# Optimization experiments

Measured on AMD Instinct MI355X. Metric: run time of the kernel, lower is better.

## Reference

```python
import jax, jax.numpy as jnp
import numpy as np
from jax import lax

B_, L_, H_, P_ = 4, 8192, 1024, 64  # batch, seq, d_model, d_state//4
EPS = 1e-5


def setup_inputs() -> dict:
    key = jax.random.key(0)
    ks = jax.random.split(key, 20)
    s = 1.0 / np.sqrt(H_)
    inp = {
        "zH": jax.random.normal(ks[0], (B_, L_, H_), jnp.float32),
        "zL": jax.random.normal(ks[1], (B_, L_, H_), jnp.float32),
        "x": jax.random.normal(ks[2], (B_, L_, H_), jnp.float32),
        "t": jax.random.normal(ks[3], (B_, H_), jnp.float32),
        # AdaLN projections (d_model -> 2*d_model)
        "W_projH": jax.random.normal(ks[4], (H_, 2 * H_), jnp.float32) * s,
        "b_projH": jnp.zeros((2 * H_,), jnp.float32),
        "W_projL": jax.random.normal(ks[5], (H_, 2 * H_), jnp.float32) * s,
        "b_projL": jnp.zeros((2 * H_,), jnp.float32),
        # inj Linear (3*d_model -> d_model)
        "W_inj": jax.random.normal(ks[6], (3 * H_, H_), jnp.float32) * (1.0 / np.sqrt(3 * H_)),
        "b_inj": jnp.zeros((H_,), jnp.float32),
        # S5Dual params (diagonal complex SSM, bidirectional)
        "Lambda_re": -(0.1 + 0.4 * jax.random.uniform(ks[7], (P_,), jnp.float32)),
        "Lambda_im": jnp.pi * jnp.arange(P_, dtype=jnp.float32),
        "B_re": jax.random.normal(ks[8], (P_, H_), jnp.float32) * s,
        "B_im": jax.random.normal(ks[9], (P_, H_), jnp.float32) * s,
        "Cf_re": jax.random.normal(ks[10], (H_, P_), jnp.float32) * (1.0 / np.sqrt(P_)),
        "Cf_im": jax.random.normal(ks[11], (H_, P_), jnp.float32) * (1.0 / np.sqrt(P_)),
        "Cb_re": jax.random.normal(ks[12], (H_, P_), jnp.float32) * (1.0 / np.sqrt(P_)),
        "Cb_im": jax.random.normal(ks[13], (H_, P_), jnp.float32) * (1.0 / np.sqrt(P_)),
        "D": jax.random.normal(ks[14], (H_,), jnp.float32),
        "log_dt": jnp.log(0.001) + (jnp.log(0.1) - jnp.log(0.001)) * jax.random.uniform(ks[15], (P_,), jnp.float32),
    }
    return inp


def _adaln(x, cond, W, b):
    # x: [B,L,H], cond: [B,H]
    scale, shift = jnp.split(cond @ W + b, 2, axis=-1)
    mu = jnp.mean(x, axis=-1, keepdims=True)
    var = jnp.var(x, axis=-1, keepdims=True)
    xn = (x - mu) * lax.rsqrt(var + EPS)
    return xn * (1.0 + scale[:, None, :]) + shift[:, None, :]


def _binop(e1, e2):
    a1, b1 = e1
    a2, b2 = e2
    return a1 * a2, a2 * b1 + b2


def _s5_dual(u, Lambda_re, Lambda_im, B_re, B_im, Cf_re, Cf_im, Cb_re, Cb_im, D, log_dt):
    # u: [B,L,H] real -> [B,L,H] real. Bidirectional diagonal SSM (S5 style).
    Lam = Lambda_re + 1j * Lambda_im            # [P]
    dt = jnp.exp(log_dt)                        # [P]
    Lam_bar = jnp.exp(Lam * dt)                 # [P] ZOH discretization
    Bm = B_re + 1j * B_im                       # [P,H]
    B_bar = ((Lam_bar - 1.0) / Lam)[:, None] * Bm
    Bu = jnp.einsum('blh,ph->blp', u.astype(jnp.complex64), B_bar)  # [B,L,P]
    A = jnp.broadcast_to(Lam_bar, Bu.shape)
    xs_f = lax.associative_scan(_binop, (A, Bu), axis=1)[1]
    xs_b = jnp.flip(lax.associative_scan(_binop, (A, jnp.flip(Bu, axis=1)), axis=1)[1], axis=1)
    Cf = Cf_re + 1j * Cf_im
    Cb = Cb_re + 1j * Cb_im
    y = 2.0 * jnp.einsum('blp,hp->blh', xs_f, Cf).real \
        + 2.0 * jnp.einsum('blp,hp->blh', xs_b, Cb).real \
        + D * u
    return y


def reference(zH, zL, x, t, W_projH, b_projH, W_projL, b_projL, W_inj, b_inj,
              Lambda_re, Lambda_im, B_re, B_im, Cf_re, Cf_im, Cb_re, Cb_im, D, log_dt):
    zH = _adaln(zH, t, W_projH, b_projH)
    zL = _adaln(zL, t, W_projL, b_projL)
    h = jnp.concatenate([zH, zL, x], axis=-1)          # [B,L,3H]
    h = h @ W_inj + b_inj                              # [B,L,H]
    return _s5_dual(h, Lambda_re, Lambda_im, B_re, B_im, Cf_re, Cf_im, Cb_re, Cb_im, D, log_dt)
```

## Files before the change

kernel.cpp:

```cpp
#include <hip/hip_runtime.h>


#define LN_EPS 1e-5f

typedef __attribute__((ext_vector_type(8))) short bf16x8;
typedef __attribute__((ext_vector_type(8))) unsigned short u16x8;
typedef __attribute__((ext_vector_type(4))) float f32x4;

__device__ __forceinline__ unsigned short f2bf(float f) {
  unsigned int u = __float_as_uint(f);
  u += 0x7fffu + ((u >> 16) & 1u);
  return (unsigned short)(u >> 16);
}
__device__ __forceinline__ float bf2f(unsigned short s) {
  return __uint_as_float(((unsigned int)s) << 16);
}

__device__ __forceinline__ void gload16(const void* g, void* l) {
  __builtin_amdgcn_global_load_lds((const __attribute__((address_space(1))) void*)g,
                                   (__attribute__((address_space(3))) void*)l, 16, 0, 0);
}

__device__ __forceinline__ void phase_bar() {
  __builtin_amdgcn_sched_barrier(0);
  asm volatile("" ::: "memory");
  __builtin_amdgcn_s_barrier();
  __builtin_amdgcn_sched_barrier(0);
}

__global__ void proj_k(const float* __restrict__ t,
                       const float* __restrict__ WH, const float* __restrict__ bH,
                       const float* __restrict__ WL, const float* __restrict__ bL,
                       float* __restrict__ cond) {
  const int idx = blockIdx.x * 256 + threadIdx.x;
  const int tensor = idx >> 11;
  const int j2 = idx & 2047;
  const float* W = tensor ? WL : WH;
  const float bv = tensor ? bL[j2] : bH[j2];
  float a0 = bv, a1 = bv, a2 = bv, a3 = bv;
  #pragma unroll 4
  for (int k = 0; k < 1024; ++k) {
    const float w = W[k * 2048 + j2];
    a0 += t[k] * w; a1 += t[1024 + k] * w; a2 += t[2048 + k] * w; a3 += t[3072 + k] * w;
  }
  const int which = j2 >> 10, j = j2 & 1023;
  float* c = cond + (size_t)((tensor * 2 + which) * 4) * 1024 + j;
  c[0] = a0; c[1024] = a1; c[2048] = a2; c[3072] = a3;
}

__global__ void proj_part_k(const float* __restrict__ t,
                            const float* __restrict__ WH, const float* __restrict__ WL,
                            float* __restrict__ part) {
  const int bid = blockIdx.x;
  const int tensor = bid >> 7, ks = (bid >> 3) & 15, jc = bid & 7;
  const int j2 = jc * 256 + threadIdx.x;
  const float* W = tensor ? WL : WH;
  float a0 = 0.f, a1 = 0.f, a2 = 0.f, a3 = 0.f;
  const int k0 = ks * 64;
  #pragma unroll 4
  for (int k = k0; k < k0 + 64; ++k) {
    const float w = W[k * 2048 + j2];
    a0 += t[k] * w; a1 += t[1024 + k] * w; a2 += t[2048 + k] * w; a3 += t[3072 + k] * w;
  }
  float* p = part + ((size_t)(tensor * 16 + ks) * 4) * 2048 + j2;
  p[0] = a0; p[2048] = a1; p[4096] = a2; p[6144] = a3;
}

__global__ void proj_red_k(const float* __restrict__ part,
                           const float* __restrict__ bH, const float* __restrict__ bL,
                           float* __restrict__ cond) {
  const int idx = blockIdx.x * 256 + threadIdx.x;
  const int tensor = idx >> 13, b = (idx >> 11) & 3, j2 = idx & 2047;
  float s = tensor ? bL[j2] : bH[j2];
  #pragma unroll
  for (int ks = 0; ks < 16; ++ks)
    s += part[((size_t)(tensor * 16 + ks) * 4 + b) * 2048 + j2];
  const int which = j2 >> 10, j = j2 & 1023;
  cond[((size_t)(tensor * 2 + which) * 4 + b) * 1024 + j] = s;
}

__global__ void transpose_winj(const float* __restrict__ W, unsigned short* __restrict__ WT) {
  __shared__ float tl[64][65];
  const int kt = blockIdx.x >> 4, nt = blockIdx.x & 15;
  const int k0 = kt << 6, n0 = nt << 6;
  const int tid = threadIdx.x;
  #pragma unroll
  for (int s = 0; s < 4; ++s) {
    const int i = s * 256 + tid;
    const int r = i >> 4, c4 = i & 15;
    const float4 v = *(const float4*)&W[(size_t)(k0 + r) * 1024 + n0 + c4 * 4];
    tl[c4 * 4 + 0][r] = v.x; tl[c4 * 4 + 1][r] = v.y;
    tl[c4 * 4 + 2][r] = v.z; tl[c4 * 4 + 3][r] = v.w;
  }
  __syncthreads();
  const int i = tid >> 2, j0 = (tid & 3) << 4;
  u16x8 w0, w1;
  #pragma unroll
  for (int q = 0; q < 8; ++q) w0[q] = f2bf(tl[i][j0 + q]);
  #pragma unroll
  for (int q = 0; q < 8; ++q) w1[q] = f2bf(tl[i][j0 + 8 + q]);
  *(u16x8*)&WT[(size_t)(n0 + i) * 3072 + k0 + j0] = w0;
  *(u16x8*)&WT[(size_t)(n0 + i) * 3072 + k0 + j0 + 8] = w1;
}

__global__ void wbu_k(const float* __restrict__ Lre, const float* __restrict__ Lim,
                      const float* __restrict__ logdt,
                      const float* __restrict__ Bre, const float* __restrict__ Bim,
                      unsigned short* __restrict__ WBuT) {
  const int idx = blockIdx.x * 256 + threadIdx.x;
  const int j = idx >> 10, hh = idx & 1023;
  const int p = j >> 1, im = j & 1;
  const float lr = Lre[p], li = Lim[p];
  const float dt = expf(logdt[p]);
  const float e = expf(lr * dt);
  float sn, cs; sincosf(li * dt, &sn, &cs);
  const float ar = e * cs - 1.f, ai = e * sn;
  const float den = lr * lr + li * li;
  const float cr = (ar * lr + ai * li) / den;
  const float ci = (ai * lr - ar * li) / den;
  const float br = Bre[p * 1024 + hh], bi = Bim[p * 1024 + hh];
  const float v = im ? (cr * bi + ci * br) : (cr * br - ci * bi);
  WBuT[idx] = f2bf(v);
}

__global__ void w2_k(const float* __restrict__ Cfre, const float* __restrict__ Cfim,
                     const float* __restrict__ Cbre, const float* __restrict__ Cbim,
                     unsigned short* __restrict__ W2T) {
  const int idx = blockIdx.x * 256 + threadIdx.x;
  const int h = idx >> 8, k = idx & 255;
  const int p = (k & 127) >> 1, im = k & 1, bw = k >> 7;
  const float* Cre = bw ? Cbre : Cfre;
  const float* Cim = bw ? Cbim : Cfim;
  const float v = im ? (-2.f * Cim[h * 64 + p]) : (2.f * Cre[h * 64 + p]);
  W2T[idx] = f2bf(v);
}

__global__ __launch_bounds__(256) void adaln_k(const float* __restrict__ zH,
                                               const float* __restrict__ zL,
                                               const float* __restrict__ x,
                                               const float* __restrict__ cond,
                                               unsigned short* __restrict__ znH,
                                               unsigned short* __restrict__ znL,
                                               unsigned short* __restrict__ xbf) {
  const int row = blockIdx.x;
  const int b = row >> 13;
  const int tid = threadIdx.x;
  const size_t rbase = (size_t)row * 1024;
  const float4 vH = *(const float4*)&zH[rbase + tid * 4];
  const float4 vL = *(const float4*)&zL[rbase + tid * 4];
  float sH = vH.x + vH.y + vH.z + vH.w;
  float qH = vH.x * vH.x + vH.y * vH.y + vH.z * vH.z + vH.w * vH.w;
  float sL = vL.x + vL.y + vL.z + vL.w;
  float qL = vL.x * vL.x + vL.y * vL.y + vL.z * vL.z + vL.w * vL.w;
  #pragma unroll
  for (int m = 1; m < 64; m <<= 1) {
    sH += __shfl_xor(sH, m); qH += __shfl_xor(qH, m);
    sL += __shfl_xor(sL, m); qL += __shfl_xor(qL, m);
  }
  __shared__ float red[4][4];
  const int wv = tid >> 6, ln = tid & 63;
  if (ln == 0) { red[wv][0] = sH; red[wv][1] = qH; red[wv][2] = sL; red[wv][3] = qL; }
  __syncthreads();
  sH = red[0][0] + red[1][0] + red[2][0] + red[3][0];
  qH = red[0][1] + red[1][1] + red[2][1] + red[3][1];
  sL = red[0][2] + red[1][2] + red[2][2] + red[3][2];
  qL = red[0][3] + red[1][3] + red[2][3] + red[3][3];
  const float muH = sH * (1.f / 1024.f);
  const float rsH = rsqrtf(qH * (1.f / 1024.f) - muH * muH + LN_EPS);
  const float muL = sL * (1.f / 1024.f);
  const float rsL = rsqrtf(qL * (1.f / 1024.f) - muL * muL + LN_EPS);
  const int h0 = tid * 4;
  const float4 scH = *(const float4*)&cond[(size_t)((0 * 2 + 0) * 4 + b) * 1024 + h0];
  const float4 shH = *(const float4*)&cond[(size_t)((0 * 2 + 1) * 4 + b) * 1024 + h0];
  const float4 scL = *(const float4*)&cond[(size_t)((1 * 2 + 0) * 4 + b) * 1024 + h0];
  const float4 shL = *(const float4*)&cond[(size_t)((1 * 2 + 1) * 4 + b) * 1024 + h0];
  ushort4 oH, oL;
  oH.x = f2bf((vH.x - muH) * rsH * (1.f + scH.x) + shH.x);
  oH.y = f2bf((vH.y - muH) * rsH * (1.f + scH.y) + shH.y);
  oH.z = f2bf((vH.z - muH) * rsH * (1.f + scH.z) + shH.z);
  oH.w = f2bf((vH.w - muH) * rsH * (1.f + scH.w) + shH.w);
  oL.x = f2bf((vL.x - muL) * rsL * (1.f + scL.x) + shL.x);
  oL.y = f2bf((vL.y - muL) * rsL * (1.f + scL.y) + shL.y);
  oL.z = f2bf((vL.z - muL) * rsL * (1.f + scL.z) + shL.z);
  oL.w = f2bf((vL.w - muL) * rsL * (1.f + scL.w) + shL.w);
  *(ushort4*)&znH[rbase + h0] = oH;
  *(ushort4*)&znL[rbase + h0] = oL;
  if (xbf != nullptr) {
    const float4 vx = *(const float4*)&x[rbase + h0];
    ushort4 ox;
    ox.x = f2bf(vx.x); ox.y = f2bf(vx.y); ox.z = f2bf(vx.z); ox.w = f2bf(vx.w);
    *(ushort4*)&xbf[rbase + h0] = ox;
  }
}

__global__ __launch_bounds__(512, 2) void gemm8p_k(
    const unsigned short* __restrict__ znH, const unsigned short* __restrict__ znL,
    const unsigned short* __restrict__ xbf, const unsigned short* __restrict__ WinjT,
    const float* __restrict__ binj, unsigned short* __restrict__ hout) {
  __shared__ char lds[131072];
  const int tid = threadIdx.x;
  const int ln = tid & 63;
  const int w = tid >> 6;
  const int wm = w >> 2, wn = w & 3;
  const int l15 = ln & 15, l4 = ln >> 4;
  const int swz = (blockIdx.x & 7) * 64 + (blockIdx.x >> 3);
  const int r0 = (swz >> 2) << 8, n0 = (swz & 3) << 8;
  constexpr int NT = 48;

  auto stageA = [&](int tau, int hf) {
    const int pidx = tau >> 4;
    const unsigned short* plane = pidx == 0 ? znH : (pidx == 1 ? znL : xbf);
    const int kbase = (tau & 15) << 6;
    char* dst0 = lds + (tau & 1) * 65536 + hf * 16384;
    #pragma unroll
    for (int i = 0; i < 2; ++i) {
      const int idx = i * 512 + tid;
      const int rl = idx >> 3, ps = idx & 7;
      const int ls = ps ^ (rl & 7);
      const unsigned short* src = plane + (size_t)(r0 + hf * 128 + rl) * 1024 + kbase + ls * 8;
      gload16(src, dst0 + i * 8192 + ((tid & 0x1C0) << 4));
    }
  };
  auto stageB = [&](int tau, int hf) {
    char* dst0 = lds + (tau & 1) * 65536 + 32768 + hf * 16384;
    #pragma unroll
    for (int i = 0; i < 2; ++i) {
      const int idx = i * 512 + tid;
      const int rl = idx >> 3, ps = idx & 7;
      const int ls = ps ^ (rl & 7);
      const unsigned short* src = WinjT + (size_t)(n0 + hf * 128 + rl) * 3072 + tau * 64 + ls * 8;
      gload16(src, dst0 + i * 8192 + ((tid & 0x1C0) << 4));
    }
  };
  auto ldA = [&](int tau, int m, int kk) -> bf16x8 {
    const int row = wm * 128 + m * 16 + l15;
    const int ps = (kk * 4 + l4) ^ (row & 7);
    return *(const bf16x8*)(lds + (tau & 1) * 65536 + row * 128 + ps * 16);
  };
  auto ldB = [&](int tau, int n, int kk) -> bf16x8 {
    const int row = wn * 64 + n * 16 + l15;
    const int ps = (kk * 4 + l4) ^ (row & 7);
    return *(const bf16x8*)(lds + (tau & 1) * 65536 + 32768 + row * 128 + ps * 16);
  };

  f32x4 acc[8][4];
  #pragma unroll
  for (int m = 0; m < 8; ++m)
    #pragma unroll
    for (int n = 0; n < 4; ++n)
      acc[m][n] = (f32x4){0.f, 0.f, 0.f, 0.f};

  stageA(0, 0); stageA(0, 1); stageB(0, 0); stageB(0, 1); stageA(1, 0); stageA(1, 1);
  asm volatile("s_waitcnt vmcnt(4)" ::: "memory");
  __builtin_amdgcn_s_barrier();
  __builtin_amdgcn_sched_barrier(0);

  for (int tau = 0; tau < NT; ++tau) {
    bf16x8 t0[4], c0[4], b0[4], t1[4], c1[4], b1[4];
    #pragma unroll
    for (int m = 0; m < 4; ++m) { t0[m] = ldA(tau, m, 0); c0[m] = ldA(tau, m, 1); }
    #pragma unroll
    for (int n = 0; n < 4; ++n) b0[n] = ldB(tau, n, 0);
    if (tau + 1 < NT) stageB(tau + 1, 0);
    phase_bar();
    __builtin_amdgcn_s_setprio(1);
    #pragma unroll
    for (int m = 0; m < 4; ++m)
      #pragma unroll
      for (int n = 0; n < 4; ++n)
        acc[m][n] = __builtin_amdgcn_mfma_f32_16x16x32_bf16(t0[m], b0[n], acc[m][n], 0, 0, 0);
    __builtin_amdgcn_s_setprio(0);
    phase_bar();
    #pragma unroll
    for (int m = 0; m < 4; ++m) { t1[m] = ldA(tau, 4 + m, 0); c1[m] = ldA(tau, 4 + m, 1); }
    if (tau + 1 < NT) stageB(tau + 1, 1);
    phase_bar();
    __builtin_amdgcn_s_setprio(1);
    #pragma unroll
    for (int m = 0; m < 4; ++m)
      #pragma unroll
      for (int n = 0; n < 4; ++n)
        acc[4 + m][n] = __builtin_amdgcn_mfma_f32_16x16x32_bf16(t1[m], b0[n], acc[4 + m][n], 0, 0, 0);
    __builtin_amdgcn_s_setprio(0);
    asm volatile("s_waitcnt lgkmcnt(0)" ::: "memory");
    phase_bar();
    #pragma unroll
    for (int n = 0; n < 4; ++n) b1[n] = ldB(tau, n, 1);
    if (tau + 2 < NT) stageA(tau + 2, 0);
    phase_bar();
    __builtin_amdgcn_s_setprio(1);
    #pragma unroll
    for (int m = 0; m < 4; ++m)
      #pragma unroll
      for (int n = 0; n < 4; ++n)
        acc[m][n] = __builtin_amdgcn_mfma_f32_16x16x32_bf16(c0[m], b1[n], acc[m][n], 0, 0, 0);
    __builtin_amdgcn_s_setprio(0);
    phase_bar();
    if (tau + 2 < NT) stageA(tau + 2, 1);
    if (tau < NT - 2) { asm volatile("s_waitcnt vmcnt(4)" ::: "memory"); }
    else              { asm volatile("s_waitcnt vmcnt(0)" ::: "memory"); }
    phase_bar();
    __builtin_amdgcn_s_setprio(1);
    #pragma unroll
    for (int m = 0; m < 4; ++m)
      #pragma unroll
      for (int n = 0; n < 4; ++n)
        acc[4 + m][n] = __builtin_amdgcn_mfma_f32_16x16x32_bf16(c1[m], b1[n], acc[4 + m][n], 0, 0, 0);
    __builtin_amdgcn_s_setprio(0);
    phase_bar();
  }

  #pragma unroll
  for (int n = 0; n < 4; ++n) {
    const int gcol = n0 + wn * 64 + n * 16 + l15;
    const float bv = binj[gcol];
    #pragma unroll
    for (int m = 0; m < 8; ++m) {
      const int grow = r0 + wm * 128 + m * 16 + l4 * 4;
      #pragma unroll
      for (int r = 0; r < 4; ++r)
        hout[(size_t)(grow + r) * 1024 + gcol] = f2bf(acc[m][n][r] + bv);
    }
  }
}

template<int KTOT, int NTOT, int CTILES, int EPI, int AMODE>
__global__ __launch_bounds__(256, 3) void gemm_k(
    const unsigned short* __restrict__ A,
    const unsigned short* __restrict__ Bm,
    const float* __restrict__ xsrc,
    const float* __restrict__ evec,
    const unsigned short* __restrict__ hbuf,
    void* __restrict__ Cout) {
  const int tid = threadIdx.x;
  const int wv = tid >> 6, ln = tid & 63;
  const int l15 = ln & 15, l4 = ln >> 4;
  const int wr = wv >> 1, wc = wv & 1;
  const int bid = blockIdx.x;
  const int rt = bid / CTILES, ct = bid % CTILES;
  const int r0 = rt << 7, n0 = ct << 7;

  __shared__ unsigned short ldsA[128 * 32];
  __shared__ unsigned short ldsB[128 * 32];

  f32x4 acc[4][4];
  #pragma unroll
  for (int i = 0; i < 4; ++i)
    #pragma unroll
    for (int j = 0; j < 4; ++j)
      acc[i][j] = (f32x4){0.f, 0.f, 0.f, 0.f};

  for (int k0 = 0; k0 < KTOT; k0 += 32) {
    __syncthreads();
    {
      const unsigned short* bb = Bm + (size_t)n0 * KTOT + k0;
      #pragma unroll
      for (int s0 = 0; s0 < 2; ++s0) {
        const int s = wv + s0 * 4;
        const int bo = (s << 10) + (ln << 4);
        const int row = bo >> 6, inb = bo & 63;
        gload16((const char*)(bb + (size_t)row * KTOT) + inb, (char*)ldsB + (s << 10));
      }
    }
    if (AMODE == 1 && k0 >= 2048) {
      const int row = tid >> 1, kf = (tid & 1) << 4;
      const float* xp = xsrc + (size_t)(r0 + row) * 1024 + (k0 - 2048) + kf;
      const float4 v0 = *(const float4*)(xp + 0);
      const float4 v1 = *(const float4*)(xp + 4);
      const float4 v2 = *(const float4*)(xp + 8);
      const float4 v3 = *(const float4*)(xp + 12);
      u16x8 w0, w1;
      w0[0] = f2bf(v0.x); w0[1] = f2bf(v0.y); w0[2] = f2bf(v0.z); w0[3] = f2bf(v0.w);
      w0[4] = f2bf(v1.x); w0[5] = f2bf(v1.y); w0[6] = f2bf(v1.z); w0[7] = f2bf(v1.w);
      w1[0] = f2bf(v2.x); w1[1] = f2bf(v2.y); w1[2] = f2bf(v2.z); w1[3] = f2bf(v2.w);
      w1[4] = f2bf(v3.x); w1[5] = f2bf(v3.y); w1[6] = f2bf(v3.z); w1[7] = f2bf(v3.w);
      *(u16x8*)&ldsA[row * 32 + kf] = w0;
      *(u16x8*)&ldsA[row * 32 + kf + 8] = w1;
    } else {
      const unsigned short* aa;
      int astr;
      if (AMODE == 0) { aa = A + (size_t)r0 * KTOT + k0; astr = KTOT; }
      else { aa = A + (size_t)(k0 >> 10) * (32768u * 1024u) + (size_t)r0 * 1024 + (k0 & 1023); astr = 1024; }
      #pragma unroll
      for (int s0 = 0; s0 < 2; ++s0) {
        const int s = wv + s0 * 4;
        const int bo = (s << 10) + (ln << 4);
        const int row = bo >> 6, inb = bo & 63;
        gload16((const char*)(aa + (size_t)row * astr) + inb, (char*)ldsA + (s << 10));
      }
    }
    __syncthreads();
    bf16x8 af[4], bfr[4];
    #pragma unroll
    for (int i = 0; i < 4; ++i)
      af[i] = *(const bf16x8*)&ldsA[(wr * 64 + i * 16 + l15) * 32 + l4 * 8];
    #pragma unroll
    for (int j = 0; j < 4; ++j)
      bfr[j] = *(const bf16x8*)&ldsB[(wc * 64 + j * 16 + l15) * 32 + l4 * 8];
    #pragma unroll
    for (int i = 0; i < 4; ++i)
      #pragma unroll
      for (int j = 0; j < 4; ++j)
        acc[i][j] = __builtin_amdgcn_mfma_f32_16x16x32_bf16(af[i], bfr[j], acc[i][j], 0, 0, 0);
  }

  #pragma unroll
  for (int j = 0; j < 4; ++j) {
    const int gcol = n0 + wc * 64 + j * 16 + l15;
    float ev = 0.f;
    if (EPI == 1 || EPI == 3) ev = evec[gcol];
    #pragma unroll
    for (int i = 0; i < 4; ++i) {
      const int gr = r0 + wr * 64 + i * 16 + l4 * 4;
      #pragma unroll
      for (int r = 0; r < 4; ++r) {
        const size_t idx = (size_t)(gr + r) * NTOT + gcol;
        const float v = acc[i][j][r];
        if (EPI == 1)      ((unsigned short*)Cout)[idx] = f2bf(v + ev);
        else if (EPI == 2) ((float*)Cout)[idx] = v;
        else               ((float*)Cout)[idx] = v + ev * bf2f(hbuf[idx]);
      }
    }
  }
}

__global__ void scan_agg_k(const float* __restrict__ Bu, float* __restrict__ agg,
                           const float* __restrict__ Lre, const float* __restrict__ Lim,
                           const float* __restrict__ logdt) {
  const int bid = blockIdx.x;
  const int dir = bid >> 8, b = (bid >> 6) & 3, ch = bid & 63;
  const int p = threadIdx.x;
  const float dt = expf(logdt[p]);
  const float e = expf(Lre[p] * dt);
  float sn, cs; sincosf(Lim[p] * dt, &sn, &cs);
  const float ar = e * cs, ai = e * sn;
  const int l0 = ch << 7;
  const float* base = Bu + ((size_t)b * 8192 + l0) * 128 + 2 * p;
  float sr = 0.f, si = 0.f;
  for (int g = 0; g < 16; ++g) {
    float2 v[8];
    #pragma unroll
    for (int u = 0; u < 8; ++u) {
      const int i = g * 8 + u;
      const int off = dir ? (127 - i) : i;
      v[u] = *(const float2*)(base + (size_t)off * 128);
    }
    #pragma unroll
    for (int u = 0; u < 8; ++u) {
      const float nr = ar * sr - ai * si + v[u].x;
      const float ni = ar * si + ai * sr + v[u].y;
      sr = nr; si = ni;
    }
  }
  float* o = agg + (((size_t)dir * 4 + b) * 64 + ch) * 128 + 2 * p;
  o[0] = sr; o[1] = si;
}

__global__ void scan_comb_k(const float* __restrict__ agg, float* __restrict__ pre,
                            const float* __restrict__ Lre, const float* __restrict__ Lim,
                            const float* __restrict__ logdt) {
  const int dir = blockIdx.x >> 2, b = blockIdx.x & 3;
  const int p = threadIdx.x;
  const float dt = expf(logdt[p]);
  const float e = expf(Lre[p] * dt);
  float sn, cs; sincosf(Lim[p] * dt, &sn, &cs);
  float Ar = e * cs, Ai = e * sn;
  #pragma unroll
  for (int q = 0; q < 7; ++q) {
    const float nr = Ar * Ar - Ai * Ai; Ai = 2.f * Ar * Ai; Ar = nr;
  }
  const float* ab = agg + ((size_t)(dir * 4 + b) * 64) * 128 + 2 * p;
  float* pb = pre + ((size_t)(dir * 4 + b) * 64) * 128 + 2 * p;
  float sr = 0.f, si = 0.f;
  for (int g = 0; g < 8; ++g) {
    float2 v[8];
    #pragma unroll
    for (int u = 0; u < 8; ++u) {
      const int i = g * 8 + u;
      const int ch = dir ? (63 - i) : i;
      v[u] = *(const float2*)(ab + (size_t)ch * 128);
    }
    #pragma unroll
    for (int u = 0; u < 8; ++u) {
      const int i = g * 8 + u;
      const int ch = dir ? (63 - i) : i;
      pb[(size_t)ch * 128] = sr; pb[(size_t)ch * 128 + 1] = si;
      const float nr = Ar * sr - Ai * si + v[u].x;
      const float ni = Ar * si + Ai * sr + v[u].y;
      sr = nr; si = ni;
    }
  }
}

__global__ void scan_apply_k(const float* __restrict__ Bu, const float* __restrict__ pre,
                             unsigned short* __restrict__ Xcat,
                             const float* __restrict__ Lre, const float* __restrict__ Lim,
                             const float* __restrict__ logdt) {
  const int bid = blockIdx.x;
  const int dir = bid >> 8, b = (bid >> 6) & 3, ch = bid & 63;
  const int p = threadIdx.x;
  const float dt = expf(logdt[p]);
  const float e = expf(Lre[p] * dt);
  float sn, cs; sincosf(Lim[p] * dt, &sn, &cs);
  const float ar = e * cs, ai = e * sn;
  const int l0 = ch << 7;
  const float* base = Bu + ((size_t)b * 8192 + l0) * 128 + 2 * p;
  const float* pr = pre + (((size_t)dir * 4 + b) * 64 + ch) * 128 + 2 * p;
  float sr = pr[0], si = pr[1];
  unsigned short* xb = Xcat + ((size_t)b * 8192 + l0) * 256 + dir * 128 + 2 * p;
  for (int g = 0; g < 16; ++g) {
    float2 v[8];
    #pragma unroll
    for (int u = 0; u < 8; ++u) {
      const int i = g * 8 + u;
      const int off = dir ? (127 - i) : i;
      v[u] = *(const float2*)(base + (size_t)off * 128);
    }
    #pragma unroll
    for (int u = 0; u < 8; ++u) {
      const int i = g * 8 + u;
      const int off = dir ? (127 - i) : i;
      const float nr = ar * sr - ai * si + v[u].x;
      const float ni = ar * si + ai * sr + v[u].y;
      sr = nr; si = ni;
      ushort2 ov; ov.x = f2bf(sr); ov.y = f2bf(si);
      *(ushort2*)(xb + (size_t)off * 256) = ov;
    }
  }
}

extern "C" void kernel_launch(void* const* d_in, const int* in_sizes, int n_in,
                              void* d_out, int out_size, void* d_ws, size_t ws_size,
                              hipStream_t stream) {
  const float* zH    = (const float*)d_in[0];
  const float* zL    = (const float*)d_in[1];
  const float* x     = (const float*)d_in[2];
  const float* t     = (const float*)d_in[3];
  const float* WpH   = (const float*)d_in[4];
  const float* bpH   = (const float*)d_in[5];
  const float* WpL   = (const float*)d_in[6];
  const float* bpL   = (const float*)d_in[7];
  const float* Winj  = (const float*)d_in[8];
  const float* binj  = (const float*)d_in[9];
  const float* Lre   = (const float*)d_in[10];
  const float* Lim   = (const float*)d_in[11];
  const float* Bre   = (const float*)d_in[12];
  const float* Bim   = (const float*)d_in[13];
  const float* Cfre  = (const float*)d_in[14];
  const float* Cfim  = (const float*)d_in[15];
  const float* Cbre  = (const float*)d_in[16];
  const float* Cbim  = (const float*)d_in[17];
  const float* Dv    = (const float*)d_in[18];
  const float* logdt = (const float*)d_in[19];

  unsigned short* znH = (unsigned short*)d_out;
  unsigned short* znL = znH + (size_t)32768 * 1024;

  const bool FAST = ws_size >= 141950976ull;
  char* ws = (char*)d_ws;

  if (FAST) {
    unsigned short* WinjT = (unsigned short*)(ws + 0);
    unsigned short* hbuf  = (unsigned short*)(ws + 6291456);
    unsigned short* WBuT  = (unsigned short*)(ws + 73400320);
    float*          cond  = (float*)(ws + 73662464);
    float*          part  = (float*)(ws + 73793536);
    char*           U     = ws + 74842112;
    unsigned short* xbf   = (unsigned short*)U;
    float*          Bu    = (float*)(U + 0);
    float*          agg   = (float*)(U + 16777216);
    float*          pre   = (float*)(U + 17039360);
    unsigned short* Xcat  = (unsigned short*)(U + 17301504);
    unsigned short* W2T   = (unsigned short*)(U + 34078720);

    proj_part_k<<<256, 256, 0, stream>>>(t, WpH, WpL, part);
    proj_red_k<<<64, 256, 0, stream>>>(part, bpH, bpL, cond);
    transpose_winj<<<768, 256, 0, stream>>>(Winj, WinjT);
    wbu_k<<<512, 256, 0, stream>>>(Lre, Lim, logdt, Bre, Bim, WBuT);
    adaln_k<<<32768, 256, 0, stream>>>(zH, zL, x, cond, znH, znL, xbf);
    gemm8p_k<<<512, 512, 0, stream>>>(znH, znL, xbf, WinjT, binj, hbuf);
    w2_k<<<1024, 256, 0, stream>>>(Cfre, Cfim, Cbre, Cbim, W2T);
    gemm_k<1024, 128, 1, 2, 0><<<256, 256, 0, stream>>>(hbuf, WBuT, nullptr, nullptr, nullptr, Bu);
    scan_agg_k<<<512, 64, 0, stream>>>(Bu, agg, Lre, Lim, logdt);
    scan_comb_k<<<8, 64, 0, stream>>>(agg, pre, Lre, Lim, logdt);
    scan_apply_k<<<512, 64, 0, stream>>>(Bu, pre, Xcat, Lre, Lim, logdt);
    gemm_k<256, 1024, 8, 3, 0><<<2048, 256, 0, stream>>>(Xcat, W2T, nullptr, Dv, hbuf, (float*)d_out);
  } else {
    unsigned short* WinjT = (unsigned short*)ws; ws += (size_t)1024 * 3072 * 2;
    unsigned short* hbuf  = (unsigned short*)ws; ws += (size_t)32768 * 1024 * 2;
    unsigned short* WBuT  = (unsigned short*)ws; ws += (size_t)128 * 1024 * 2;
    float*          Bu    = (float*)ws;          ws += (size_t)32768 * 128 * 4;
    float*          cond  = (float*)ws;          ws += (size_t)2 * 2 * 4 * 1024 * 4;
    float*          agg   = (float*)ws;          ws += (size_t)2 * 4 * 64 * 128 * 4;
    float*          pre   = (float*)ws;          ws += (size_t)2 * 4 * 64 * 128 * 4;
    unsigned short* Xcat  = (unsigned short*)ws; ws += (size_t)32768 * 256 * 2;
    unsigned short* W2T   = (unsigned short*)ws; ws += (size_t)1024 * 256 * 2;

    proj_k<<<16, 256, 0, stream>>>(t, WpH, bpH, WpL, bpL, cond);
    transpose_winj<<<768, 256, 0, stream>>>(Winj, WinjT);
    wbu_k<<<512, 256, 0, stream>>>(Lre, Lim, logdt, Bre, Bim, WBuT);
    w2_k<<<1024, 256, 0, stream>>>(Cfre, Cfim, Cbre, Cbim, W2T);
    adaln_k<<<32768, 256, 0, stream>>>(zH, zL, x, cond, znH, znL, nullptr);
    gemm_k<3072, 1024, 8, 1, 1><<<2048, 256, 0, stream>>>(znH, WinjT, x, binj, nullptr, hbuf);
    gemm_k<1024, 128, 1, 2, 0><<<256, 256, 0, stream>>>(hbuf, WBuT, nullptr, nullptr, nullptr, Bu);
    scan_agg_k<<<512, 64, 0, stream>>>(Bu, agg, Lre, Lim, logdt);
    scan_comb_k<<<8, 64, 0, stream>>>(agg, pre, Lre, Lim, logdt);
    scan_apply_k<<<512, 64, 0, stream>>>(Bu, pre, Xcat, Lre, Lim, logdt);
    gemm_k<256, 1024, 8, 3, 0><<<2048, 256, 0, stream>>>(Xcat, W2T, nullptr, Dv, hbuf, (float*)d_out);
  }
}
```

Baseline: 433.4 us.

## Fuse weight-prep kernels and load x directly as fp32 inside the injection GEMM

Merges the Winj transpose, WBuT, W2T and projection-partial kernels into one prep kernel, which cuts the number of launches. Removes the separate bf16 copy of x written by adaln. The injection GEMM now reads fp32 x from global memory into registers for the last K-tiles, converts it to bf16 and writes it to LDS itself, and the vmcnt wait thresholds are adjusted to match. This saves a round trip of x through a bf16 buffer, at the cost of more register pressure and synchronous global loads inside the GEMM pipeline.

```diff
diff --git a/kernel.cpp b/kernel.cpp
--- a/kernel.cpp
+++ b/kernel.cpp
@@ -48,22 +48,78 @@
   c[0] = a0; c[1024] = a1; c[2048] = a2; c[3072] = a3;
 }
 
-__global__ void proj_part_k(const float* __restrict__ t,
-                            const float* __restrict__ WH, const float* __restrict__ WL,
-                            float* __restrict__ part) {
+__global__ void prep_k(const float* __restrict__ Winj, unsigned short* __restrict__ WinjT,
+                       const float* __restrict__ Lre, const float* __restrict__ Lim,
+                       const float* __restrict__ logdt,
+                       const float* __restrict__ Bre, const float* __restrict__ Bim,
+                       unsigned short* __restrict__ WBuT,
+                       const float* __restrict__ Cfre, const float* __restrict__ Cfim,
+                       const float* __restrict__ Cbre, const float* __restrict__ Cbim,
+                       unsigned short* __restrict__ W2T,
+                       const float* __restrict__ t,
+                       const float* __restrict__ WH, const float* __restrict__ WL,
+                       float* __restrict__ part) {
+  __shared__ float tl[64][65];
   const int bid = blockIdx.x;
-  const int tensor = bid >> 7, ks = (bid >> 3) & 15, jc = bid & 7;
-  const int j2 = jc * 256 + threadIdx.x;
-  const float* W = tensor ? WL : WH;
-  float a0 = 0.f, a1 = 0.f, a2 = 0.f, a3 = 0.f;
-  const int k0 = ks * 64;
-  #pragma unroll 4
-  for (int k = k0; k < k0 + 64; ++k) {
-    const float w = W[k * 2048 + j2];
-    a0 += t[k] * w; a1 += t[1024 + k] * w; a2 += t[2048 + k] * w; a3 += t[3072 + k] * w;
-  }
-  float* p = part + ((size_t)(tensor * 16 + ks) * 4) * 2048 + j2;
-  p[0] = a0; p[2048] = a1; p[4096] = a2; p[6144] = a3;
+  const int tid = threadIdx.x;
+  if (bid < 768) {
+    const int kt = bid >> 4, nt = bid & 15;
+    const int k0 = kt << 6, n0 = nt << 6;
+    #pragma unroll
+    for (int s = 0; s < 4; ++s) {
+      const int i = s * 256 + tid;
+      const int r = i >> 4, c4 = i & 15;
+      const float4 v = *(const float4*)&Winj[(size_t)(k0 + r) * 1024 + n0 + c4 * 4];
+      tl[c4 * 4 + 0][r] = v.x; tl[c4 * 4 + 1][r] = v.y;
+      tl[c4 * 4 + 2][r] = v.z; tl[c4 * 4 + 3][r] = v.w;
+    }
+    __syncthreads();
+    const int i = tid >> 2, j0 = (tid & 3) << 4;
+    u16x8 w0, w1;
+    #pragma unroll
+    for (int q = 0; q < 8; ++q) w0[q] = f2bf(tl[i][j0 + q]);
+    #pragma unroll
+    for (int q = 0; q < 8; ++q) w1[q] = f2bf(tl[i][j0 + 8 + q]);
+    *(u16x8*)&WinjT[(size_t)(n0 + i) * 3072 + k0 + j0] = w0;
+    *(u16x8*)&WinjT[(size_t)(n0 + i) * 3072 + k0 + j0 + 8] = w1;
+  } else if (bid < 1280) {
+    const int idx = (bid - 768) * 256 + tid;
+    const int j = idx >> 10, hh = idx & 1023;
+    const int p = j >> 1, im = j & 1;
+    const float lr = Lre[p], li = Lim[p];
+    const float dt = expf(logdt[p]);
+    const float e = expf(lr * dt);
+    float sn, cs; sincosf(li * dt, &sn, &cs);
+    const float ar = e * cs - 1.f, ai = e * sn;
+    const float den = lr * lr + li * li;
+    const float cr = (ar * lr + ai * li) / den;
+    const float ci = (ai * lr - ar * li) / den;
+    const float br = Bre[p * 1024 + hh], bi = Bim[p * 1024 + hh];
+    const float v = im ? (cr * bi + ci * br) : (cr * br - ci * bi);
+    WBuT[idx] = f2bf(v);
+  } else if (bid < 2304) {
+    const int idx = (bid - 1280) * 256 + tid;
+    const int h = idx >> 8, k = idx & 255;
+    const int p = (k & 127) >> 1, im = k & 1, bw = k >> 7;
+    const float* Cre = bw ? Cbre : Cfre;
+    const float* Cim = bw ? Cbim : Cfim;
+    const float v = im ? (-2.f * Cim[h * 64 + p]) : (2.f * Cre[h * 64 + p]);
+    W2T[idx] = f2bf(v);
+  } else {
+    const int pb = bid - 2304;
+    const int tensor = pb >> 7, ks = (pb >> 3) & 15, jc = pb & 7;
+    const int j2 = jc * 256 + tid;
+    const float* W = tensor ? WL : WH;
+    float a0 = 0.f, a1 = 0.f, a2 = 0.f, a3 = 0.f;
+    const int k0 = ks * 64;
+    #pragma unroll 4
+    for (int k = k0; k < k0 + 64; ++k) {
+      const float w = W[k * 2048 + j2];
+      a0 += t[k] * w; a1 += t[1024 + k] * w; a2 += t[2048 + k] * w; a3 += t[3072 + k] * w;
+    }
+    float* p = part + ((size_t)(tensor * 16 + ks) * 4) * 2048 + j2;
+    p[0] = a0; p[2048] = a1; p[4096] = a2; p[6144] = a3;
+  }
 }
 
 __global__ void proj_red_k(const float* __restrict__ part,
@@ -137,11 +193,9 @@
 
 __global__ __launch_bounds__(256) void adaln_k(const float* __restrict__ zH,
                                                const float* __restrict__ zL,
-                                               const float* __restrict__ x,
                                                const float* __restrict__ cond,
                                                unsigned short* __restrict__ znH,
-                                               unsigned short* __restrict__ znL,
-                                               unsigned short* __restrict__ xbf) {
+                                               unsigned short* __restrict__ znL) {
   const int row = blockIdx.x;
   const int b = row >> 13;
   const int tid = threadIdx.x;
@@ -185,17 +239,11 @@
   oL.w = f2bf((vL.w - muL) * rsL * (1.f + scL.w) + shL.w);
   *(ushort4*)&znH[rbase + h0] = oH;
   *(ushort4*)&znL[rbase + h0] = oL;
-  if (xbf != nullptr) {
-    const float4 vx = *(const float4*)&x[rbase + h0];
-    ushort4 ox;
-    ox.x = f2bf(vx.x); ox.y = f2bf(vx.y); ox.z = f2bf(vx.z); ox.w = f2bf(vx.w);
-    *(ushort4*)&xbf[rbase + h0] = ox;
-  }
 }
 
 __global__ __launch_bounds__(512, 2) void gemm8p_k(
     const unsigned short* __restrict__ znH, const unsigned short* __restrict__ znL,
-    const unsigned short* __restrict__ xbf, const unsigned short* __restrict__ WinjT,
+    const float* __restrict__ xsrc, const unsigned short* __restrict__ WinjT,
     const float* __restrict__ binj, unsigned short* __restrict__ hout) {
   __shared__ char lds[131072];
   const int tid = threadIdx.x;
@@ -209,7 +257,7 @@
 
   auto stageA = [&](int tau, int hf) {
     const int pidx = tau >> 4;
-    const unsigned short* plane = pidx == 0 ? znH : (pidx == 1 ? znL : xbf);
+    const unsigned short* plane = pidx == 0 ? znH : znL;
     const int kbase = (tau & 15) << 6;
     char* dst0 = lds + (tau & 1) * 65536 + hf * 16384;
     #pragma unroll
@@ -250,18 +298,35 @@
     for (int n = 0; n < 4; ++n)
       acc[m][n] = (f32x4){0.f, 0.f, 0.f, 0.f};
 
+  const int xr_rl0 = tid >> 3, xr_ls0 = (tid & 7) ^ (xr_rl0 & 7);
+  const int s1 = 512 + tid;
+  const int xr_rl1 = s1 >> 3, xr_ls1 = (s1 & 7) ^ (xr_rl1 & 7);
+  float4 xa0, xa1, xa2, xa3;
+  float4 xb0, xb1, xb2, xb3;
+
   stageA(0, 0); stageA(0, 1); stageB(0, 0); stageB(0, 1); stageA(1, 0); stageA(1, 1);
   asm volatile("s_waitcnt vmcnt(4)" ::: "memory");
   __builtin_amdgcn_s_barrier();
   __builtin_amdgcn_sched_barrier(0);
 
   for (int tau = 0; tau < NT; ++tau) {
+    const bool stg = (tau + 2 < NT) && (tau + 2 < 32);
+    const bool stx = (tau + 2 < NT) && (tau + 2 >= 32);
+    const int kx = (tau + 2 - 32) << 6;
     bf16x8 t0[4], c0[4], b0[4], t1[4], c1[4], b1[4];
     #pragma unroll
-    for (int m = 0; m < 4; ++m) { t0[m] = ldA(tau, m, 0); c0[m] = ldA(tau, m, 1); }
+    for (int m = 0; m < 4; ++m) t0[m] = ldA(tau, m, 0);
     #pragma unroll
     for (int n = 0; n < 4; ++n) b0[n] = ldB(tau, n, 0);
+    #pragma unroll
+    for (int m = 0; m < 4; ++m) c0[m] = ldA(tau, m, 1);
     if (tau + 1 < NT) stageB(tau + 1, 0);
+    if (stx) {
+      const float* xp0 = xsrc + (size_t)(r0 + xr_rl0) * 1024 + kx + xr_ls0 * 8;
+      const float* xp1 = xsrc + (size_t)(r0 + xr_rl1) * 1024 + kx + xr_ls1 * 8;
+      xa0 = *(const float4*)xp0; xa1 = *(const float4*)(xp0 + 4);
+      xa2 = *(const float4*)xp1; xa3 = *(const float4*)(xp1 + 4);
+    }
     phase_bar();
     __builtin_amdgcn_s_setprio(1);
     #pragma unroll
@@ -272,8 +337,16 @@
     __builtin_amdgcn_s_setprio(0);
     phase_bar();
     #pragma unroll
-    for (int m = 0; m < 4; ++m) { t1[m] = ldA(tau, 4 + m, 0); c1[m] = ldA(tau, 4 + m, 1); }
+    for (int m = 0; m < 4; ++m) t1[m] = ldA(tau, 4 + m, 0);
+    #pragma unroll
+    for (int m = 0; m < 4; ++m) c1[m] = ldA(tau, 4 + m, 1);
     if (tau + 1 < NT) stageB(tau + 1, 1);
+    if (stx) {
+      const float* xp0 = xsrc + (size_t)(r0 + 128 + xr_rl0) * 1024 + kx + xr_ls0 * 8;
+      const float* xp1 = xsrc + (size_t)(r0 + 128 + xr_rl1) * 1024 + kx + xr_ls1 * 8;
+      xb0 = *(const float4*)xp0; xb1 = *(const float4*)(xp0 + 4);
+      xb2 = *(const float4*)xp1; xb3 = *(const float4*)(xp1 + 4);
+    }
     phase_bar();
     __builtin_amdgcn_s_setprio(1);
     #pragma unroll
@@ -286,7 +359,17 @@
     phase_bar();
     #pragma unroll
     for (int n = 0; n < 4; ++n) b1[n] = ldB(tau, n, 1);
-    if (tau + 2 < NT) stageA(tau + 2, 0);
+    if (stg) stageA(tau + 2, 0);
+    else if (stx) {
+      char* dst0 = lds + (tau & 1) * 65536;
+      u16x8 w0, w1;
+      w0[0] = f2bf(xa0.x); w0[1] = f2bf(xa0.y); w0[2] = f2bf(xa0.z); w0[3] = f2bf(xa0.w);
+      w0[4] = f2bf(xa1.x); w0[5] = f2bf(xa1.y); w0[6] = f2bf(xa1.z); w0[7] = f2bf(xa1.w);
+      w1[0] = f2bf(xa2.x); w1[1] = f2bf(xa2.y); w1[2] = f2bf(xa2.z); w1[3] = f2bf(xa2.w);
+      w1[4] = f2bf(xa3.x); w1[5] = f2bf(xa3.y); w1[6] = f2bf(xa3.z); w1[7] = f2bf(xa3.w);
+      *(u16x8*)(dst0 + tid * 16) = w0;
+      *(u16x8*)(dst0 + (512 + tid) * 16) = w1;
+    }
     phase_bar();
     __builtin_amdgcn_s_setprio(1);
     #pragma unroll
@@ -296,9 +379,19 @@
         acc[m][n] = __builtin_amdgcn_mfma_f32_16x16x32_bf16(c0[m], b1[n], acc[m][n], 0, 0, 0);
     __builtin_amdgcn_s_setprio(0);
     phase_bar();
-    if (tau + 2 < NT) stageA(tau + 2, 1);
-    if (tau < NT - 2) { asm volatile("s_waitcnt vmcnt(4)" ::: "memory"); }
-    else              { asm volatile("s_waitcnt vmcnt(0)" ::: "memory"); }
+    if (stg) stageA(tau + 2, 1);
+    else if (stx) {
+      char* dst0 = lds + (tau & 1) * 65536 + 16384;
+      u16x8 w0, w1;
+      w0[0] = f2bf(xb0.x); w0[1] = f2bf(xb0.y); w0[2] = f2bf(xb0.z); w0[3] = f2bf(xb0.w);
+      w0[4] = f2bf(xb1.x); w0[5] = f2bf(xb1.y); w0[6] = f2bf(xb1.z); w0[7] = f2bf(xb1.w);
+      w1[0] = f2bf(xb2.x); w1[1] = f2bf(xb2.y); w1[2] = f2bf(xb2.z); w1[3] = f2bf(xb2.w);
+      w1[4] = f2bf(xb3.x); w1[5] = f2bf(xb3.y); w1[6] = f2bf(xb3.z); w1[7] = f2bf(xb3.w);
+      *(u16x8*)(dst0 + tid * 16) = w0;
+      *(u16x8*)(dst0 + (512 + tid) * 16) = w1;
+    }
+    if (tau < 30) { asm volatile("s_waitcnt vmcnt(4)" ::: "memory"); }
+    else          { asm volatile("s_waitcnt vmcnt(0)" ::: "memory"); }
     phase_bar();
     __builtin_amdgcn_s_setprio(1);
     #pragma unroll
@@ -566,20 +659,17 @@
     float*          cond  = (float*)(ws + 73662464);
     float*          part  = (float*)(ws + 73793536);
     char*           U     = ws + 74842112;
-    unsigned short* xbf   = (unsigned short*)U;
     float*          Bu    = (float*)(U + 0);
     float*          agg   = (float*)(U + 16777216);
     float*          pre   = (float*)(U + 17039360);
     unsigned short* Xcat  = (unsigned short*)(U + 17301504);
     unsigned short* W2T   = (unsigned short*)(U + 34078720);
 
-    proj_part_k<<<256, 256, 0, stream>>>(t, WpH, WpL, part);
+    prep_k<<<2560, 256, 0, stream>>>(Winj, WinjT, Lre, Lim, logdt, Bre, Bim, WBuT,
+                                     Cfre, Cfim, Cbre, Cbim, W2T, t, WpH, WpL, part);
     proj_red_k<<<64, 256, 0, stream>>>(part, bpH, bpL, cond);
-    transpose_winj<<<768, 256, 0, stream>>>(Winj, WinjT);
-    wbu_k<<<512, 256, 0, stream>>>(Lre, Lim, logdt, Bre, Bim, WBuT);
-    adaln_k<<<32768, 256, 0, stream>>>(zH, zL, x, cond, znH, znL, xbf);
-    gemm8p_k<<<512, 512, 0, stream>>>(znH, znL, xbf, WinjT, binj, hbuf);
-    w2_k<<<1024, 256, 0, stream>>>(Cfre, Cfim, Cbre, Cbim, W2T);
+    adaln_k<<<32768, 256, 0, stream>>>(zH, zL, cond, znH, znL);
+    gemm8p_k<<<512, 512, 0, stream>>>(znH, znL, x, WinjT, binj, hbuf);
     gemm_k<1024, 128, 1, 2, 0><<<256, 256, 0, stream>>>(hbuf, WBuT, nullptr, nullptr, nullptr, Bu);
     scan_agg_k<<<512, 64, 0, stream>>>(Bu, agg, Lre, Lim, logdt);
     scan_comb_k<<<8, 64, 0, stream>>>(agg, pre, Lre, Lim, logdt);
@@ -600,7 +690,7 @@
     transpose_winj<<<768, 256, 0, stream>>>(Winj, WinjT);
     wbu_k<<<512, 256, 0, stream>>>(Lre, Lim, logdt, Bre, Bim, WBuT);
     w2_k<<<1024, 256, 0, stream>>>(Cfre, Cfim, Cbre, Cbim, W2T);
-    adaln_k<<<32768, 256, 0, stream>>>(zH, zL, x, cond, znH, znL, nullptr);
+    adaln_k<<<32768, 256, 0, stream>>>(zH, zL, cond, znH, znL);
     gemm_k<3072, 1024, 8, 1, 1><<<2048, 256, 0, stream>>>(znH, WinjT, x, binj, nullptr, hbuf);
     gemm_k<1024, 128, 1, 2, 0><<<256, 256, 0, stream>>>(hbuf, WBuT, nullptr, nullptr, nullptr, Bu);
     scan_agg_k<<<512, 64, 0, stream>>>(Bu, agg, Lre, Lim, logdt);
```

After: 501.1 us. 15.6% more time.

## Merge prep kernels into one launch and fold scan combine into apply

Applied to the files above, without the earlier changes.

Three small setup kernels (W_inj transpose, B_bar weight build, AdaLN projection partials) become one launch that branches on block index. The separate chunk-prefix combine kernel is removed: each apply block recomputes its own carry-in by serially folding the preceding chunk aggregates with Lambda_bar^128. This drops two kernel launches and the inter-kernel gaps, at the cost of redundant serial prefix work per block (up to 63 steps).

```diff
diff --git a/kernel.cpp b/kernel.cpp
--- a/kernel.cpp
+++ b/kernel.cpp
@@ -48,22 +48,67 @@
   c[0] = a0; c[1024] = a1; c[2048] = a2; c[3072] = a3;
 }
 
-__global__ void proj_part_k(const float* __restrict__ t,
-                            const float* __restrict__ WH, const float* __restrict__ WL,
-                            float* __restrict__ part) {
+__global__ void prep_k(const float* __restrict__ Winj, unsigned short* __restrict__ WinjT,
+                       const float* __restrict__ Lre, const float* __restrict__ Lim,
+                       const float* __restrict__ logdt,
+                       const float* __restrict__ Bre, const float* __restrict__ Bim,
+                       unsigned short* __restrict__ WBuT,
+                       const float* __restrict__ t,
+                       const float* __restrict__ WH, const float* __restrict__ WL,
+                       float* __restrict__ part) {
+  __shared__ float tl[64][65];
   const int bid = blockIdx.x;
-  const int tensor = bid >> 7, ks = (bid >> 3) & 15, jc = bid & 7;
-  const int j2 = jc * 256 + threadIdx.x;
-  const float* W = tensor ? WL : WH;
-  float a0 = 0.f, a1 = 0.f, a2 = 0.f, a3 = 0.f;
-  const int k0 = ks * 64;
-  #pragma unroll 4
-  for (int k = k0; k < k0 + 64; ++k) {
-    const float w = W[k * 2048 + j2];
-    a0 += t[k] * w; a1 += t[1024 + k] * w; a2 += t[2048 + k] * w; a3 += t[3072 + k] * w;
-  }
-  float* p = part + ((size_t)(tensor * 16 + ks) * 4) * 2048 + j2;
-  p[0] = a0; p[2048] = a1; p[4096] = a2; p[6144] = a3;
+  const int tid = threadIdx.x;
+  if (bid < 768) {
+    const int kt = bid >> 4, nt = bid & 15;
+    const int k0 = kt << 6, n0 = nt << 6;
+    #pragma unroll
+    for (int s = 0; s < 4; ++s) {
+      const int i = s * 256 + tid;
+      const int r = i >> 4, c4 = i & 15;
+      const float4 v = *(const float4*)&Winj[(size_t)(k0 + r) * 1024 + n0 + c4 * 4];
+      tl[c4 * 4 + 0][r] = v.x; tl[c4 * 4 + 1][r] = v.y;
+      tl[c4 * 4 + 2][r] = v.z; tl[c4 * 4 + 3][r] = v.w;
+    }
+    __syncthreads();
+    const int i = tid >> 2, j0 = (tid & 3) << 4;
+    u16x8 w0, w1;
+    #pragma unroll
+    for (int q = 0; q < 8; ++q) w0[q] = f2bf(tl[i][j0 + q]);
+    #pragma unroll
+    for (int q = 0; q < 8; ++q) w1[q] = f2bf(tl[i][j0 + 8 + q]);
+    *(u16x8*)&WinjT[(size_t)(n0 + i) * 3072 + k0 + j0] = w0;
+    *(u16x8*)&WinjT[(size_t)(n0 + i) * 3072 + k0 + j0 + 8] = w1;
+  } else if (bid < 1280) {
+    const int idx = (bid - 768) * 256 + tid;
+    const int j = idx >> 10, hh = idx & 1023;
+    const int p = j >> 1, im = j & 1;
+    const float lr = Lre[p], li = Lim[p];
+    const float dt = expf(logdt[p]);
+    const float e = expf(lr * dt);
+    float sn, cs; sincosf(li * dt, &sn, &cs);
+    const float ar = e * cs - 1.f, ai = e * sn;
+    const float den = lr * lr + li * li;
+    const float cr = (ar * lr + ai * li) / den;
+    const float ci = (ai * lr - ar * li) / den;
+    const float br = Bre[p * 1024 + hh], bi = Bim[p * 1024 + hh];
+    const float v = im ? (cr * bi + ci * br) : (cr * br - ci * bi);
+    WBuT[idx] = f2bf(v);
+  } else {
+    const int pb = bid - 1280;
+    const int tensor = pb >> 7, ks = (pb >> 3) & 15, jc = pb & 7;
+    const int j2 = jc * 256 + tid;
+    const float* W = tensor ? WL : WH;
+    float a0 = 0.f, a1 = 0.f, a2 = 0.f, a3 = 0.f;
+    const int k0 = ks * 64;
+    #pragma unroll 4
+    for (int k = k0; k < k0 + 64; ++k) {
+      const float w = W[k * 2048 + j2];
+      a0 += t[k] * w; a1 += t[1024 + k] * w; a2 += t[2048 + k] * w; a3 += t[3072 + k] * w;
+    }
+    float* p = part + ((size_t)(tensor * 16 + ks) * 4) * 2048 + j2;
+    p[0] = a0; p[2048] = a1; p[4096] = a2; p[6144] = a3;
+  }
 }
 
 __global__ void proj_red_k(const float* __restrict__ part,
@@ -529,6 +574,63 @@
   }
 }
 
+__global__ void scan_apply2_k(const float* __restrict__ Bu, const float* __restrict__ agg,
+                              unsigned short* __restrict__ Xcat,
+                              const float* __restrict__ Lre, const float* __restrict__ Lim,
+                              const float* __restrict__ logdt) {
+  const int bid = blockIdx.x;
+  const int dir = bid >> 8, b = (bid >> 6) & 3, ch = bid & 63;
+  const int p = threadIdx.x;
+  const float dt = expf(logdt[p]);
+  const float e = expf(Lre[p] * dt);
+  float sn, cs; sincosf(Lim[p] * dt, &sn, &cs);
+  const float ar = e * cs, ai = e * sn;
+  float Ar = ar, Ai = ai;
+  #pragma unroll
+  for (int q = 0; q < 7; ++q) {
+    const float nr = Ar * Ar - Ai * Ai; Ai = 2.f * Ar * Ai; Ar = nr;
+  }
+  const float* ab = agg + ((size_t)(dir * 4 + b) * 64) * 128 + 2 * p;
+  float sr = 0.f, si = 0.f;
+  const int nk = dir ? (63 - ch) : ch;
+  for (int g0 = 0; g0 < nk; g0 += 8) {
+    const int gn = (nk - g0) < 8 ? (nk - g0) : 8;
+    float2 v[8];
+    for (int u = 0; u < gn; ++u) {
+      const int i = g0 + u;
+      const int k = dir ? (63 - i) : i;
+      v[u] = *(const float2*)(ab + (size_t)k * 128);
+    }
+    for (int u = 0; u < gn; ++u) {
+      const float nr = Ar * sr - Ai * si + v[u].x;
+      const float ni = Ar * si + Ai * sr + v[u].y;
+      sr = nr; si = ni;
+    }
+  }
+  const int l0 = ch << 7;
+  const float* base = Bu + ((size_t)b * 8192 + l0) * 128 + 2 * p;
+  unsigned short* xb = Xcat + ((size_t)b * 8192 + l0) * 256 + dir * 128 + 2 * p;
+  for (int g = 0; g < 16; ++g) {
+    float2 v[8];
+    #pragma unroll
+    for (int u = 0; u < 8; ++u) {
+      const int i = g * 8 + u;
+      const int off = dir ? (127 - i) : i;
+      v[u] = *(const float2*)(base + (size_t)off * 128);
+    }
+    #pragma unroll
+    for (int u = 0; u < 8; ++u) {
+      const int i = g * 8 + u;
+      const int off = dir ? (127 - i) : i;
+      const float nr = ar * sr - ai * si + v[u].x;
+      const float ni = ar * si + ai * sr + v[u].y;
+      sr = nr; si = ni;
+      ushort2 ov; ov.x = f2bf(sr); ov.y = f2bf(si);
+      *(ushort2*)(xb + (size_t)off * 256) = ov;
+    }
+  }
+}
+
 extern "C" void kernel_launch(void* const* d_in, const int* in_sizes, int n_in,
                               void* d_out, int out_size, void* d_ws, size_t ws_size,
                               hipStream_t stream) {
@@ -569,21 +671,18 @@
     unsigned short* xbf   = (unsigned short*)U;
     float*          Bu    = (float*)(U + 0);
     float*          agg   = (float*)(U + 16777216);
-    float*          pre   = (float*)(U + 17039360);
     unsigned short* Xcat  = (unsigned short*)(U + 17301504);
     unsigned short* W2T   = (unsigned short*)(U + 34078720);
 
-    proj_part_k<<<256, 256, 0, stream>>>(t, WpH, WpL, part);
+    prep_k<<<1536, 256, 0, stream>>>(Winj, WinjT, Lre, Lim, logdt, Bre, Bim, WBuT,
+                                     t, WpH, WpL, part);
     proj_red_k<<<64, 256, 0, stream>>>(part, bpH, bpL, cond);
-    transpose_winj<<<768, 256, 0, stream>>>(Winj, WinjT);
-    wbu_k<<<512, 256, 0, stream>>>(Lre, Lim, logdt, Bre, Bim, WBuT);
     adaln_k<<<32768, 256, 0, stream>>>(zH, zL, x, cond, znH, znL, xbf);
     gemm8p_k<<<512, 512, 0, stream>>>(znH, znL, xbf, WinjT, binj, hbuf);
     w2_k<<<1024, 256, 0, stream>>>(Cfre, Cfim, Cbre, Cbim, W2T);
     gemm_k<1024, 128, 1, 2, 0><<<256, 256, 0, stream>>>(hbuf, WBuT, nullptr, nullptr, nullptr, Bu);
     scan_agg_k<<<512, 64, 0, stream>>>(Bu, agg, Lre, Lim, logdt);
-    scan_comb_k<<<8, 64, 0, stream>>>(agg, pre, Lre, Lim, logdt);
-    scan_apply_k<<<512, 64, 0, stream>>>(Bu, pre, Xcat, Lre, Lim, logdt);
+    scan_apply2_k<<<512, 64, 0, stream>>>(Bu, agg, Xcat, Lre, Lim, logdt);
     gemm_k<256, 1024, 8, 3, 0><<<2048, 256, 0, stream>>>(Xcat, W2T, nullptr, Dv, hbuf, (float*)d_out);
   } else {
     unsigned short* WinjT = (unsigned short*)ws; ws += (size_t)1024 * 3072 * 2;
```

After: 451.3 us. +4.1%, slower.
